# Performance work log

Hardware: AMD Instinct MI355X
Metric: run time of the kernel (lower is better)

## Reference

```python
import jax, jax.numpy as jnp
import numpy as np

N_NODES = 50000
N_EDGES = 1600000
IN_DIM = 128
N_HEADS = 8
OUT_DIM = 16  # output_dim // n_heads = 128 // 8


def setup_inputs() -> dict:
    key = jax.random.key(0)
    ks = jax.random.split(key, 8)
    feature = jax.random.normal(ks[0], (N_NODES, IN_DIM), dtype=jnp.float32)
    edge_src = jax.random.randint(ks[1], (N_EDGES,), 0, N_NODES)
    edge_dst = jax.random.randint(ks[2], (N_EDGES,), 0, N_NODES)
    edge_weight = jax.random.uniform(ks[3], (N_EDGES,), dtype=jnp.float32)
    w_lin = jax.random.normal(ks[4], (IN_DIM, N_HEADS * OUT_DIM), dtype=jnp.float32) * 0.1
    att_l = jax.random.normal(ks[5], (N_HEADS, OUT_DIM), dtype=jnp.float32) * 0.1
    att_r = jax.random.normal(ks[6], (N_HEADS, OUT_DIM), dtype=jnp.float32) * 0.1
    w_res = jax.random.normal(ks[7], (IN_DIM, N_HEADS * OUT_DIM), dtype=jnp.float32) * 0.1
    return {"feature": feature, "edge_src": edge_src, "edge_dst": edge_dst,
            "edge_weight": edge_weight, "w_lin": w_lin, "att_l": att_l,
            "att_r": att_r, "w_res": w_res}


def reference(feature, edge_src, edge_dst, edge_weight, w_lin, att_l, att_r, w_res):
    N = feature.shape[0]
    H, C = att_l.shape
    # Linear projection -> [N, H, C]
    x = (feature @ w_lin).reshape(N, H, C)
    # Per-node attention logits [N, H]
    al = jnp.einsum('nhc,hc->nh', x, att_l)
    ar = jnp.einsum('nhc,hc->nh', x, att_r)
    # Per-edge logits: gather src/dst, weight, leaky-relu  [E, H]
    alpha = al[edge_src] + ar[edge_dst]
    alpha = edge_weight[:, None] * alpha
    alpha = jax.nn.leaky_relu(alpha, negative_slope=0.2)
    # Segment softmax over edges grouped by destination node
    m = jax.ops.segment_max(alpha, edge_dst, num_segments=N)  # [N, H]
    m = jnp.where(jnp.isfinite(m), m, 0.0)
    e = jnp.exp(alpha - m[edge_dst])
    denom = jax.ops.segment_sum(e, edge_dst, num_segments=N)  # [N, H]
    coef = e / denom[edge_dst]                                 # [E, H]
    # Message passing: gather src feats, weight by coef, scatter-sum to dst
    msg = x[edge_src] * coef[:, :, None]                       # [E, H, C]
    feat = jax.ops.segment_sum(msg, edge_dst, num_segments=N)  # [N, H, C]
    out = jax.nn.elu(feat).reshape(N, H * C)
    out = out + feature @ w_res  # residual branch
    return out
```

## Files before the change

### kernel.cpp

```cpp
#include <hip/hip_runtime.h>
#include <math.h>

#define IN_DIM 128
#define NH 8
#define OC 16
#define HC 128
#define BSTR 136
#define ECH 4096
#define NBINS_MAX 512

typedef __attribute__((ext_vector_type(8))) short short8;
typedef __attribute__((ext_vector_type(4))) float f32x4;

__device__ __forceinline__ unsigned short bf16_rne(float f) {
  unsigned int u = __builtin_bit_cast(unsigned int, f);
  u += 0x7FFFu + ((u >> 16) & 1u);
  return (unsigned short)(u >> 16);
}
__device__ __forceinline__ float bf16_to_f(unsigned short h) {
  unsigned int u = ((unsigned int)h) << 16;
  return __builtin_bit_cast(float, u);
}

__global__ __launch_bounds__(256) void k1_fused(const float* __restrict__ feature,
                                                const float* __restrict__ w_lin,
                                                const float* __restrict__ w_res,
                                                unsigned short* __restrict__ xbf,
                                                float* __restrict__ out, int N) {
  __shared__ unsigned short BL[HC * BSTR];
  __shared__ unsigned short BR[HC * BSTR];
  const int t = threadIdx.x;
  for (int i = t; i < IN_DIM * HC; i += 256) {
    const int r = i >> 7, c = i & 127;
    BL[c * BSTR + r] = bf16_rne(w_lin[i]);
    BR[c * BSTR + r] = bf16_rne(w_res[i]);
  }
  __syncthreads();

  const int wave = t >> 6, lane = t & 63;
  const int n16 = lane & 15, quad = lane >> 4;
  const int nStrips = (N + 15) >> 4;

  for (int strip = blockIdx.x * 4 + wave; strip < nStrips; strip += gridDim.x * 4) {
    const int row0 = strip * 16;
    const int arow = row0 + n16;
    const float* __restrict__ ap =
        feature + (size_t)((arow < N) ? arow : 0) * IN_DIM + quad * 8;
    short8 ahi[4], alo[4];
#pragma unroll
    for (int ks = 0; ks < 4; ++ks) {
      const float4 f0 = *(const float4*)(ap + ks * 32);
      const float4 f1 = *(const float4*)(ap + ks * 32 + 4);
      const float fv[8] = {f0.x, f0.y, f0.z, f0.w, f1.x, f1.y, f1.z, f1.w};
      short8 h, l;
#pragma unroll
      for (int j = 0; j < 8; ++j) {
        const unsigned short hh = bf16_rne(fv[j]);
        h[j] = (short)hh;
        l[j] = (short)bf16_rne(fv[j] - bf16_to_f(hh));
      }
      ahi[ks] = h;
      alo[ks] = l;
    }
#pragma unroll
    for (int cg = 0; cg < 2; ++cg) {
      f32x4 acc[4] = {{0.f,0.f,0.f,0.f},{0.f,0.f,0.f,0.f},{0.f,0.f,0.f,0.f},{0.f,0.f,0.f,0.f}};
#pragma unroll
      for (int ks = 0; ks < 4; ++ks) {
#pragma unroll
        for (int j = 0; j < 4; ++j) {
          const int boff = ((cg * 4 + j) * 16 + n16) * BSTR + ks * 32 + quad * 8;
          const short8 bh = *(const short8*)&BL[boff];
          acc[j] = __builtin_amdgcn_mfma_f32_16x16x32_bf16(ahi[ks], bh, acc[j], 0, 0, 0);
          acc[j] = __builtin_amdgcn_mfma_f32_16x16x32_bf16(alo[ks], bh, acc[j], 0, 0, 0);
        }
      }
#pragma unroll
      for (int j = 0; j < 4; ++j) {
        const int colo = (cg * 4 + j) * 16 + n16;
#pragma unroll
        for (int r = 0; r < 4; ++r) {
          const int rr = row0 + quad * 4 + r;
          if (rr < N) xbf[(size_t)rr * HC + colo] = bf16_rne(acc[j][r]);
        }
      }
    }
#pragma unroll
    for (int cg = 0; cg < 2; ++cg) {
      f32x4 acc[4] = {{0.f,0.f,0.f,0.f},{0.f,0.f,0.f,0.f},{0.f,0.f,0.f,0.f},{0.f,0.f,0.f,0.f}};
#pragma unroll
      for (int ks = 0; ks < 4; ++ks) {
#pragma unroll
        for (int j = 0; j < 4; ++j) {
          const int boff = ((cg * 4 + j) * 16 + n16) * BSTR + ks * 32 + quad * 8;
          const short8 bh = *(const short8*)&BR[boff];
          acc[j] = __builtin_amdgcn_mfma_f32_16x16x32_bf16(ahi[ks], bh, acc[j], 0, 0, 0);
          acc[j] = __builtin_amdgcn_mfma_f32_16x16x32_bf16(alo[ks], bh, acc[j], 0, 0, 0);
        }
      }
#pragma unroll
      for (int j = 0; j < 4; ++j) {
        const int colo = (cg * 4 + j) * 16 + n16;
#pragma unroll
        for (int r = 0; r < 4; ++r) {
          const int rr = row0 + quad * 4 + r;
          if (rr < N) out[(size_t)rr * HC + colo] = acc[j][r];
        }
      }
    }
  }
}

__global__ __launch_bounds__(256) void k1b_attn(const unsigned short* __restrict__ xbf,
                                                const float* __restrict__ att_l,
                                                const float* __restrict__ att_r,
                                                float* __restrict__ al,
                                                float* __restrict__ ar,
                                                unsigned char* __restrict__ x8,
                                                float* __restrict__ s, int N) {
  const int idx = blockIdx.x * 256 + threadIdx.x;
  if (idx >= N * NH) return;
  const int h = idx & (NH - 1);
  const int n = idx >> 3;
  const ushort4* xp = (const ushort4*)(xbf + (size_t)idx * OC);
  const float4* lp = (const float4*)(att_l + h * OC);
  const float4* rp = (const float4*)(att_r + h * OC);
  float f[16];
  float sl = 0.f, sr = 0.f, m = 0.f;
#pragma unroll
  for (int q = 0; q < 4; ++q) {
    const ushort4 xu = xp[q];
    const float4 lv = lp[q], rv = rp[q];
    f[q * 4 + 0] = bf16_to_f(xu.x);
    f[q * 4 + 1] = bf16_to_f(xu.y);
    f[q * 4 + 2] = bf16_to_f(xu.z);
    f[q * 4 + 3] = bf16_to_f(xu.w);
    sl += f[q*4+0] * lv.x + f[q*4+1] * lv.y + f[q*4+2] * lv.z + f[q*4+3] * lv.w;
    sr += f[q*4+0] * rv.x + f[q*4+1] * rv.y + f[q*4+2] * rv.z + f[q*4+3] * rv.w;
#pragma unroll
    for (int j = 0; j < 4; ++j) m = fmaxf(m, fabsf(f[q * 4 + j]));
  }
  al[idx] = sl;
  ar[idx] = sr;
  m = fmaxf(m, __shfl_xor(m, 1, 64));
  m = fmaxf(m, __shfl_xor(m, 2, 64));
  m = fmaxf(m, __shfl_xor(m, 4, 64));
  const float inv = (m > 0.f) ? 127.f / m : 0.f;
  int4 pk;
  unsigned* pw = (unsigned*)&pk;
#pragma unroll
  for (int w = 0; w < 4; ++w) {
    unsigned b0 = (unsigned)((int)rintf(f[w * 4 + 0] * inv) + 128);
    unsigned b1 = (unsigned)((int)rintf(f[w * 4 + 1] * inv) + 128);
    unsigned b2 = (unsigned)((int)rintf(f[w * 4 + 2] * inv) + 128);
    unsigned b3 = (unsigned)((int)rintf(f[w * 4 + 3] * inv) + 128);
    pw[w] = (b0 & 0xFFu) | ((b1 & 0xFFu) << 8) | ((b2 & 0xFFu) << 16) | ((b3 & 0xFFu) << 24);
  }
  *(int4*)(x8 + (size_t)n * HC + h * 16) = pk;
  if (h == 0) s[n] = (m > 0.f) ? m / 127.f : 0.f;
}

__global__ __launch_bounds__(256) void kb1_scatter(const int* __restrict__ esrc,
                                                   const int* __restrict__ edst,
                                                   const float* __restrict__ ew,
                                                   int* __restrict__ bin_cursor,
                                                   uint2* __restrict__ tmp,
                                                   int E, int nbins, int cap) {
  __shared__ int cnt[NBINS_MAX];
  __shared__ int gbase[NBINS_MAX];
  const int t = threadIdx.x;
  cnt[t] = 0;
  cnt[t + 256] = 0;
  __syncthreads();
  const int base = blockIdx.x * ECH;
  uint2 v[16];
  int bj[16], sj[16];
#pragma unroll
  for (int j = 0; j < 16; ++j) {
    const int e = base + j * 256 + t;
    bj[j] = -1;
    if (e < E) {
      const int d = edst[e];
      v[j] = make_uint2((unsigned)esrc[e] | ((unsigned)(d & 127) << 16),
                        __float_as_uint(ew[e]));
      bj[j] = d >> 7;
      sj[j] = atomicAdd(&cnt[bj[j]], 1);
    }
  }
  __syncthreads();
  for (int b = t; b < nbins; b += 256) {
    const int own = cnt[b];
    if (own > 0) gbase[b] = atomicAdd(&bin_cursor[b], own);
  }
  __syncthreads();
#pragma unroll
  for (int j = 0; j < 16; ++j)
    if (bj[j] >= 0) {
      const int p = gbase[bj[j]] + sj[j];
      if (p < cap) tmp[(size_t)bj[j] * cap + p] = v[j];
    }
}

__global__ __launch_bounds__(512) void kb2_scan(const int* __restrict__ bin_cursor,
                                                int* __restrict__ bin_ofs,
                                                int* __restrict__ row_start,
                                                int nbins, int N) {
  __shared__ int s[512];
  const int t = threadIdx.x;
  const int own = (t < nbins) ? bin_cursor[t] : 0;
  s[t] = own;
  __syncthreads();
  for (int o = 1; o < 512; o <<= 1) {
    const int a = (t >= o) ? s[t - o] : 0;
    __syncthreads();
    s[t] += a;
    __syncthreads();
  }
  if (t < nbins) bin_ofs[t] = s[t] - own;
  if (t == nbins - 1) {
    bin_ofs[nbins] = s[t];
    row_start[N] = s[t];
  }
}

__global__ __launch_bounds__(256) void kb3_sort(const uint2* __restrict__ tmp,
                                                const int* __restrict__ bin_cursor,
                                                const int* __restrict__ bin_ofs,
                                                uint2* __restrict__ packed,
                                                int* __restrict__ row_start,
                                                int cap, int N) {
  const int b = blockIdx.x, t = threadIdx.x;
  const int M = bin_cursor[b];
  const int gstart = bin_ofs[b];
  const uint2* __restrict__ src = tmp + (size_t)b * cap;
  __shared__ int cnt[128];
  __shared__ int cur[128];
  __shared__ int s[128];
  if (t < 128) cnt[t] = 0;
  __syncthreads();
  for (int i = t; i < M; i += 256) atomicAdd(&cnt[src[i].x >> 16], 1);
  __syncthreads();
  if (t < 128) s[t] = cnt[t];
  __syncthreads();
  for (int o = 1; o < 128; o <<= 1) {
    int a = 0;
    if (t < 128 && t >= o) a = s[t - o];
    __syncthreads();
    if (t < 128) s[t] += a;
    __syncthreads();
  }
  if (t < 128) {
    const int ex = s[t] - cnt[t];
    cur[t] = gstart + ex;
    const int node = b * 128 + t;
    if (node < N) row_start[node] = gstart + ex;
  }
  __syncthreads();
  for (int i = t; i < M; i += 256) {
    const uint2 v = src[i];
    const int pos = atomicAdd(&cur[v.x >> 16], 1);
    packed[pos] = make_uint2(v.x & 0xFFFFu, v.y);
  }
}

__global__ __launch_bounds__(64) void k5_agg(const unsigned char* __restrict__ x8,
                                             const float* __restrict__ s,
                                             const uint2* __restrict__ packed,
                                             const int* __restrict__ row_start,
                                             const float* __restrict__ al,
                                             const float* __restrict__ ar,
                                             float* __restrict__ out, int N) {
  const int n = blockIdx.x;
  const int l = threadIdx.x;
  const int s0 = row_start[n];
  const int En = row_start[n + 1] - s0;
  if (En == 0) return;
  __shared__ int sbuf[64];
  __shared__ float wbuf[64];
  __shared__ float scbuf[64];
  const int h = l & 7;
  const int g = l >> 3;
  const int ch0 = h * 16;

  const float arn = ar[(size_t)n * NH + h];
  float dpart = 0.f;
  float facsum = 0.f;
  float f[16];
#pragma unroll
  for (int j = 0; j < 16; ++j) f[j] = 0.f;

  for (int base = 0; base < En; base += 64) {
    const int cnt = min(64, En - base);
    __syncthreads();
    if (l < cnt) {
      const uint2 p = packed[s0 + base + l];
      const int src = (int)p.x;
      sbuf[l] = src;
      wbuf[l] = __uint_as_float(p.y);
      scbuf[l] = s[src];
    }
    __syncthreads();
    for (int i = g; i < cnt; i += 8) {
      const int src = sbuf[i];
      float a = wbuf[i] * (al[(size_t)src * NH + h] + arn);
      a = (a > 0.f) ? a : 0.2f * a;
      const float e = __expf(a);
      dpart += e;
      const float fac = e * scbuf[i];
      facsum += fac;
      const int4 qw = *(const int4*)(x8 + (size_t)src * HC + ch0);
      const unsigned ux = (unsigned)qw.x, uy = (unsigned)qw.y;
      const unsigned uz = (unsigned)qw.z, uw = (unsigned)qw.w;
      f[0]  = fmaf(fac, (float)(ux & 0xFFu),         f[0]);
      f[1]  = fmaf(fac, (float)((ux >> 8) & 0xFFu),  f[1]);
      f[2]  = fmaf(fac, (float)((ux >> 16) & 0xFFu), f[2]);
      f[3]  = fmaf(fac, (float)(ux >> 24),           f[3]);
      f[4]  = fmaf(fac, (float)(uy & 0xFFu),         f[4]);
      f[5]  = fmaf(fac, (float)((uy >> 8) & 0xFFu),  f[5]);
      f[6]  = fmaf(fac, (float)((uy >> 16) & 0xFFu), f[6]);
      f[7]  = fmaf(fac, (float)(uy >> 24),           f[7]);
      f[8]  = fmaf(fac, (float)(uz & 0xFFu),         f[8]);
      f[9]  = fmaf(fac, (float)((uz >> 8) & 0xFFu),  f[9]);
      f[10] = fmaf(fac, (float)((uz >> 16) & 0xFFu), f[10]);
      f[11] = fmaf(fac, (float)(uz >> 24),           f[11]);
      f[12] = fmaf(fac, (float)(uw & 0xFFu),         f[12]);
      f[13] = fmaf(fac, (float)((uw >> 8) & 0xFFu),  f[13]);
      f[14] = fmaf(fac, (float)((uw >> 16) & 0xFFu), f[14]);
      f[15] = fmaf(fac, (float)(uw >> 24),           f[15]);
    }
  }
  dpart += __shfl_xor(dpart, 8);
  dpart += __shfl_xor(dpart, 16);
  dpart += __shfl_xor(dpart, 32);
  facsum += __shfl_xor(facsum, 8);
  facsum += __shfl_xor(facsum, 16);
  facsum += __shfl_xor(facsum, 32);
  const float inv = 1.f / dpart;
#pragma unroll
  for (int j = 0; j < 16; ++j) {
    f[j] += __shfl_xor(f[j], 8);
    f[j] += __shfl_xor(f[j], 16);
    f[j] += __shfl_xor(f[j], 32);
  }
  if (g == 0) {
    float* __restrict__ outp = out + (size_t)n * HC + ch0;
#pragma unroll
    for (int j = 0; j < 16; ++j) {
      const float feat = (f[j] - 128.f * facsum) * inv;
      const float o = (feat > 0.f) ? feat : (__expf(feat) - 1.f);
      outp[j] += o;
    }
  }
}

extern "C" void kernel_launch(void* const* d_in, const int* in_sizes, int n_in,
                              void* d_out, int out_size, void* d_ws, size_t ws_size,
                              hipStream_t stream) {
  const float* feature = (const float*)d_in[0];
  const int* esrc = (const int*)d_in[1];
  const int* edst = (const int*)d_in[2];
  const float* ew = (const float*)d_in[3];
  const float* w_lin = (const float*)d_in[4];
  const float* att_l = (const float*)d_in[5];
  const float* att_r = (const float*)d_in[6];
  const float* w_res = (const float*)d_in[7];
  float* out = (float*)d_out;

  const int N = in_sizes[0] / IN_DIM;
  const int E = in_sizes[1];
  const int nbins = (N + 127) >> 7;
  int cap = (E + nbins - 1) / nbins;
  cap = cap + cap / 4 + 512;
  cap = (cap + 63) & ~63;
  const int nch = (E + ECH - 1) / ECH;

  char* ws = (char*)d_ws;
  size_t off = 0;
  auto alloc = [&](size_t bytes) {
    void* p = ws + off;
    off = (off + bytes + 255) & ~(size_t)255;
    return p;
  };
  const size_t xbf_bytes = (size_t)N * HC * sizeof(unsigned short);
  const size_t tmp_bytes = (size_t)nbins * cap * sizeof(uint2);
  void* region0 = alloc(tmp_bytes > xbf_bytes ? tmp_bytes : xbf_bytes);
  unsigned short* xbf = (unsigned short*)region0;
  uint2* tmp = (uint2*)region0;

  unsigned char* x8 = (unsigned char*)alloc((size_t)N * HC);
  float* sscale = (float*)alloc((size_t)N * sizeof(float));
  float* al = (float*)alloc((size_t)N * NH * sizeof(float));
  float* ar = (float*)alloc((size_t)N * NH * sizeof(float));
  int* row_start = (int*)alloc((size_t)(N + 1) * sizeof(int));
  int* bin_cursor = (int*)alloc((size_t)NBINS_MAX * sizeof(int));
  int* bin_ofs = (int*)alloc((size_t)(NBINS_MAX + 1) * sizeof(int));
  uint2* packed = (uint2*)alloc((size_t)E * sizeof(uint2));

  hipMemsetAsync(bin_cursor, 0, (size_t)NBINS_MAX * sizeof(int), stream);
  k1_fused<<<512, 256, 0, stream>>>(feature, w_lin, w_res, xbf, out, N);
  k1b_attn<<<(N * NH + 255) / 256, 256, 0, stream>>>(xbf, att_l, att_r, al, ar, x8, sscale, N);
  kb1_scatter<<<nch, 256, 0, stream>>>(esrc, edst, ew, bin_cursor, tmp, E, nbins, cap);
  kb2_scan<<<1, 512, 0, stream>>>(bin_cursor, bin_ofs, row_start, nbins, N);
  kb3_sort<<<nbins, 256, 0, stream>>>(tmp, bin_cursor, bin_ofs, packed, row_start, cap, N);
  k5_agg<<<N, 64, 0, stream>>>(x8, sscale, packed, row_start, al, ar, out, N);
}
```

Before: 223.9 us.

## Fuse attention logits and int8 quantization into GEMM kernel, drop scan and memset launches

The projection GEMM now computes the per-node attention logits and the per-node int8 quantization straight from the MFMA accumulators, so the bf16 intermediate and the separate attention kernel go away. The bin-cursor memset moves into block 0 of the GEMM kernel. The single-block scan kernel is replaced by each sort block summing the preceding bin counts itself. The aggregation epilogue now reduces partial sums through shared memory and writes float2 vectors instead of using shuffles and a single-group store. Together this removes several launches and an HBM round trip, at the cost of more shuffles in the GEMM and redundant prefix sums in the sort kernel. The memset now relies on the GEMM kernel finishing before the scatter kernel starts.

```diff
diff --git a/kernel.cpp b/kernel.cpp
--- a/kernel.cpp
+++ b/kernel.cpp
@@ -8,6 +8,7 @@
 #define BSTR 136
 #define ECH 4096
 #define NBINS_MAX 512
+#define FSTR 132
 
 typedef __attribute__((ext_vector_type(8))) short short8;
 typedef __attribute__((ext_vector_type(4))) float f32x4;
@@ -25,11 +26,21 @@
 __global__ __launch_bounds__(256) void k1_fused(const float* __restrict__ feature,
                                                 const float* __restrict__ w_lin,
                                                 const float* __restrict__ w_res,
-                                                unsigned short* __restrict__ xbf,
-                                                float* __restrict__ out, int N) {
+                                                const float* __restrict__ att_l,
+                                                const float* __restrict__ att_r,
+                                                unsigned char* __restrict__ x8,
+                                                float* __restrict__ sscale,
+                                                float* __restrict__ al,
+                                                float* __restrict__ ar,
+                                                float* __restrict__ out,
+                                                int* __restrict__ bin_cursor, int N) {
   __shared__ unsigned short BL[HC * BSTR];
   __shared__ unsigned short BR[HC * BSTR];
   const int t = threadIdx.x;
+  if (blockIdx.x == 0) {
+    bin_cursor[t] = 0;
+    bin_cursor[t + 256] = 0;
+  }
   for (int i = t; i < IN_DIM * HC; i += 256) {
     const int r = i >> 7, c = i & 127;
     BL[c * BSTR + r] = bf16_rne(w_lin[i]);
@@ -39,6 +50,12 @@
 
   const int wave = t >> 6, lane = t & 63;
   const int n16 = lane & 15, quad = lane >> 4;
+  float attl[8], attr[8];
+#pragma unroll
+  for (int hh = 0; hh < 8; ++hh) {
+    attl[hh] = att_l[hh * OC + n16];
+    attr[hh] = att_r[hh * OC + n16];
+  }
   const int nStrips = (N + 15) >> 4;
 
   for (int strip = blockIdx.x * 4 + wave; strip < nStrips; strip += gridDim.x * 4) {
@@ -62,26 +79,62 @@
       ahi[ks] = h;
       alo[ks] = l;
     }
-#pragma unroll
-    for (int cg = 0; cg < 2; ++cg) {
-      f32x4 acc[4] = {{0.f,0.f,0.f,0.f},{0.f,0.f,0.f,0.f},{0.f,0.f,0.f,0.f},{0.f,0.f,0.f,0.f}};
-#pragma unroll
-      for (int ks = 0; ks < 4; ++ks) {
-#pragma unroll
-        for (int j = 0; j < 4; ++j) {
-          const int boff = ((cg * 4 + j) * 16 + n16) * BSTR + ks * 32 + quad * 8;
-          const short8 bh = *(const short8*)&BL[boff];
-          acc[j] = __builtin_amdgcn_mfma_f32_16x16x32_bf16(ahi[ks], bh, acc[j], 0, 0, 0);
-          acc[j] = __builtin_amdgcn_mfma_f32_16x16x32_bf16(alo[ks], bh, acc[j], 0, 0, 0);
+    f32x4 xacc[8];
+#pragma unroll
+    for (int u = 0; u < 8; ++u) xacc[u] = (f32x4){0.f, 0.f, 0.f, 0.f};
+#pragma unroll
+    for (int ks = 0; ks < 4; ++ks) {
+#pragma unroll
+      for (int u = 0; u < 8; ++u) {
+        const int boff = (u * 16 + n16) * BSTR + ks * 32 + quad * 8;
+        const short8 bh = *(const short8*)&BL[boff];
+        xacc[u] = __builtin_amdgcn_mfma_f32_16x16x32_bf16(ahi[ks], bh, xacc[u], 0, 0, 0);
+        xacc[u] = __builtin_amdgcn_mfma_f32_16x16x32_bf16(alo[ks], bh, xacc[u], 0, 0, 0);
+      }
+    }
+    float m[4];
+#pragma unroll
+    for (int r = 0; r < 4; ++r) {
+      float mm = 0.f;
+#pragma unroll
+      for (int u = 0; u < 8; ++u) mm = fmaxf(mm, fabsf(xacc[u][r]));
+      mm = fmaxf(mm, __shfl_xor(mm, 1));
+      mm = fmaxf(mm, __shfl_xor(mm, 2));
+      mm = fmaxf(mm, __shfl_xor(mm, 4));
+      mm = fmaxf(mm, __shfl_xor(mm, 8));
+      m[r] = mm;
+    }
+#pragma unroll
+    for (int r = 0; r < 4; ++r) {
+      const int rr = row0 + quad * 4 + r;
+      if (rr < N) {
+        const float inv = (m[r] > 0.f) ? 127.f / m[r] : 0.f;
+#pragma unroll
+        for (int u = 0; u < 8; ++u) {
+          const int q8 = (int)rintf(xacc[u][r] * inv) + 128;
+          x8[(size_t)rr * HC + u * 16 + n16] = (unsigned char)q8;
         }
-      }
-#pragma unroll
-      for (int j = 0; j < 4; ++j) {
-        const int colo = (cg * 4 + j) * 16 + n16;
-#pragma unroll
-        for (int r = 0; r < 4; ++r) {
-          const int rr = row0 + quad * 4 + r;
-          if (rr < N) xbf[(size_t)rr * HC + colo] = bf16_rne(acc[j][r]);
+        if (n16 == 0) sscale[rr] = (m[r] > 0.f) ? m[r] / 127.f : 0.f;
+      }
+    }
+#pragma unroll
+    for (int u = 0; u < 8; ++u) {
+#pragma unroll
+      for (int r = 0; r < 4; ++r) {
+        float tl = xacc[u][r] * attl[u];
+        float tr = xacc[u][r] * attr[u];
+        tl += __shfl_xor(tl, 1);
+        tr += __shfl_xor(tr, 1);
+        tl += __shfl_xor(tl, 2);
+        tr += __shfl_xor(tr, 2);
+        tl += __shfl_xor(tl, 4);
+        tr += __shfl_xor(tr, 4);
+        tl += __shfl_xor(tl, 8);
+        tr += __shfl_xor(tr, 8);
+        const int rr = row0 + quad * 4 + r;
+        if (n16 == 0 && rr < N) {
+          al[(size_t)rr * NH + u] = tl;
+          ar[(size_t)rr * NH + u] = tr;
         }
       }
     }
@@ -109,55 +162,6 @@
       }
     }
   }
-}
-
-__global__ __launch_bounds__(256) void k1b_attn(const unsigned short* __restrict__ xbf,
-                                                const float* __restrict__ att_l,
-                                                const float* __restrict__ att_r,
-                                                float* __restrict__ al,
-                                                float* __restrict__ ar,
-                                                unsigned char* __restrict__ x8,
-                                                float* __restrict__ s, int N) {
-  const int idx = blockIdx.x * 256 + threadIdx.x;
-  if (idx >= N * NH) return;
-  const int h = idx & (NH - 1);
-  const int n = idx >> 3;
-  const ushort4* xp = (const ushort4*)(xbf + (size_t)idx * OC);
-  const float4* lp = (const float4*)(att_l + h * OC);
-  const float4* rp = (const float4*)(att_r + h * OC);
-  float f[16];
-  float sl = 0.f, sr = 0.f, m = 0.f;
-#pragma unroll
-  for (int q = 0; q < 4; ++q) {
-    const ushort4 xu = xp[q];
-    const float4 lv = lp[q], rv = rp[q];
-    f[q * 4 + 0] = bf16_to_f(xu.x);
-    f[q * 4 + 1] = bf16_to_f(xu.y);
-    f[q * 4 + 2] = bf16_to_f(xu.z);
-    f[q * 4 + 3] = bf16_to_f(xu.w);
-    sl += f[q*4+0] * lv.x + f[q*4+1] * lv.y + f[q*4+2] * lv.z + f[q*4+3] * lv.w;
-    sr += f[q*4+0] * rv.x + f[q*4+1] * rv.y + f[q*4+2] * rv.z + f[q*4+3] * rv.w;
-#pragma unroll
-    for (int j = 0; j < 4; ++j) m = fmaxf(m, fabsf(f[q * 4 + j]));
-  }
-  al[idx] = sl;
-  ar[idx] = sr;
-  m = fmaxf(m, __shfl_xor(m, 1, 64));
-  m = fmaxf(m, __shfl_xor(m, 2, 64));
-  m = fmaxf(m, __shfl_xor(m, 4, 64));
-  const float inv = (m > 0.f) ? 127.f / m : 0.f;
-  int4 pk;
-  unsigned* pw = (unsigned*)&pk;
-#pragma unroll
-  for (int w = 0; w < 4; ++w) {
-    unsigned b0 = (unsigned)((int)rintf(f[w * 4 + 0] * inv) + 128);
-    unsigned b1 = (unsigned)((int)rintf(f[w * 4 + 1] * inv) + 128);
-    unsigned b2 = (unsigned)((int)rintf(f[w * 4 + 2] * inv) + 128);
-    unsigned b3 = (unsigned)((int)rintf(f[w * 4 + 3] * inv) + 128);
-    pw[w] = (b0 & 0xFFu) | ((b1 & 0xFFu) << 8) | ((b2 & 0xFFu) << 16) | ((b3 & 0xFFu) << 24);
-  }
-  *(int4*)(x8 + (size_t)n * HC + h * 16) = pk;
-  if (h == 0) s[n] = (m > 0.f) ? m / 127.f : 0.f;
 }
 
 __global__ __launch_bounds__(256) void kb1_scatter(const int* __restrict__ esrc,
@@ -197,41 +201,27 @@
   for (int j = 0; j < 16; ++j)
     if (bj[j] >= 0) {
       const int p = gbase[bj[j]] + sj[j];
-      if (p < cap) tmp[(size_t)bj[j] * cap + p] = v[j];
-    }
-}
-
-__global__ __launch_bounds__(512) void kb2_scan(const int* __restrict__ bin_cursor,
-                                                int* __restrict__ bin_ofs,
-                                                int* __restrict__ row_start,
-                                                int nbins, int N) {
-  __shared__ int s[512];
-  const int t = threadIdx.x;
-  const int own = (t < nbins) ? bin_cursor[t] : 0;
-  s[t] = own;
-  __syncthreads();
-  for (int o = 1; o < 512; o <<= 1) {
-    const int a = (t >= o) ? s[t - o] : 0;
-    __syncthreads();
-    s[t] += a;
-    __syncthreads();
-  }
-  if (t < nbins) bin_ofs[t] = s[t] - own;
-  if (t == nbins - 1) {
-    bin_ofs[nbins] = s[t];
-    row_start[N] = s[t];
-  }
+      if (p >= 0 && p < cap) tmp[(size_t)bj[j] * cap + p] = v[j];
+    }
 }
 
 __global__ __launch_bounds__(256) void kb3_sort(const uint2* __restrict__ tmp,
                                                 const int* __restrict__ bin_cursor,
-                                                const int* __restrict__ bin_ofs,
                                                 uint2* __restrict__ packed,
                                                 int* __restrict__ row_start,
-                                                int cap, int N) {
+                                                int cap, int nbins, int N) {
   const int b = blockIdx.x, t = threadIdx.x;
   const int M = bin_cursor[b];
-  const int gstart = bin_ofs[b];
+  __shared__ int redw[4];
+  int part = 0;
+  for (int i = t; i < b; i += 256) part += bin_cursor[i];
+#pragma unroll
+  for (int o = 32; o >= 1; o >>= 1) part += __shfl_xor(part, o);
+  if ((t & 63) == 0) redw[t >> 6] = part;
+  __syncthreads();
+  const int gstart = redw[0] + redw[1] + redw[2] + redw[3];
+  if (b == nbins - 1 && t == 0) row_start[N] = gstart + M;
+
   const uint2* __restrict__ src = tmp + (size_t)b * cap;
   __shared__ int cnt[128];
   __shared__ int cur[128];
@@ -278,6 +268,7 @@
   __shared__ int sbuf[64];
   __shared__ float wbuf[64];
   __shared__ float scbuf[64];
+  __shared__ float fred[8 * FSTR];
   const int h = l & 7;
   const int g = l >> 3;
   const int ch0 = h * 16;
@@ -335,22 +326,30 @@
   facsum += __shfl_xor(facsum, 8);
   facsum += __shfl_xor(facsum, 16);
   facsum += __shfl_xor(facsum, 32);
-  const float inv = 1.f / dpart;
-#pragma unroll
-  for (int j = 0; j < 16; ++j) {
-    f[j] += __shfl_xor(f[j], 8);
-    f[j] += __shfl_xor(f[j], 16);
-    f[j] += __shfl_xor(f[j], 32);
-  }
-  if (g == 0) {
-    float* __restrict__ outp = out + (size_t)n * HC + ch0;
-#pragma unroll
-    for (int j = 0; j < 16; ++j) {
-      const float feat = (f[j] - 128.f * facsum) * inv;
-      const float o = (feat > 0.f) ? feat : (__expf(feat) - 1.f);
-      outp[j] += o;
-    }
-  }
+#pragma unroll
+  for (int q = 0; q < 4; ++q) {
+    const f32x4 v = {f[q * 4 + 0], f[q * 4 + 1], f[q * 4 + 2], f[q * 4 + 3]};
+    *(f32x4*)&fred[g * FSTR + ch0 + q * 4] = v;
+  }
+  __syncthreads();
+  float a0 = 0.f, a1 = 0.f;
+#pragma unroll
+  for (int gg = 0; gg < 8; ++gg) {
+    const float2 v = *(const float2*)&fred[gg * FSTR + 2 * l];
+    a0 += v.x;
+    a1 += v.y;
+  }
+  const float dH = __shfl(dpart, l >> 3);
+  const float fsH = __shfl(facsum, l >> 3);
+  const float inv = 1.f / dH;
+  float f0 = (a0 - 128.f * fsH) * inv;
+  float f1 = (a1 - 128.f * fsH) * inv;
+  f0 = (f0 > 0.f) ? f0 : (__expf(f0) - 1.f);
+  f1 = (f1 > 0.f) ? f1 : (__expf(f1) - 1.f);
+  float2 o = *(float2*)&out[(size_t)n * HC + 2 * l];
+  o.x += f0;
+  o.y += f1;
+  *(float2*)&out[(size_t)n * HC + 2 * l] = o;
 }
 
 extern "C" void kernel_launch(void* const* d_in, const int* in_sizes, int n_in,
@@ -381,26 +380,18 @@
     off = (off + bytes + 255) & ~(size_t)255;
     return p;
   };
-  const size_t xbf_bytes = (size_t)N * HC * sizeof(unsigned short);
-  const size_t tmp_bytes = (size_t)nbins * cap * sizeof(uint2);
-  void* region0 = alloc(tmp_bytes > xbf_bytes ? tmp_bytes : xbf_bytes);
-  unsigned short* xbf = (unsigned short*)region0;
-  uint2* tmp = (uint2*)region0;
-
+  uint2* tmp = (uint2*)alloc((size_t)nbins * cap * sizeof(uint2));
   unsigned char* x8 = (unsigned char*)alloc((size_t)N * HC);
   float* sscale = (float*)alloc((size_t)N * sizeof(float));
   float* al = (float*)alloc((size_t)N * NH * sizeof(float));
   float* ar = (float*)alloc((size_t)N * NH * sizeof(float));
   int* row_start = (int*)alloc((size_t)(N + 1) * sizeof(int));
   int* bin_cursor = (int*)alloc((size_t)NBINS_MAX * sizeof(int));
-  int* bin_ofs = (int*)alloc((size_t)(NBINS_MAX + 1) * sizeof(int));
   uint2* packed = (uint2*)alloc((size_t)E * sizeof(uint2));
 
-  hipMemsetAsync(bin_cursor, 0, (size_t)NBINS_MAX * sizeof(int), stream);
-  k1_fused<<<512, 256, 0, stream>>>(feature, w_lin, w_res, xbf, out, N);
-  k1b_attn<<<(N * NH + 255) / 256, 256, 0, stream>>>(xbf, att_l, att_r, al, ar, x8, sscale, N);
+  k1_fused<<<512, 256, 0, stream>>>(feature, w_lin, w_res, att_l, att_r,
+                                    x8, sscale, al, ar, out, bin_cursor, N);
   kb1_scatter<<<nch, 256, 0, stream>>>(esrc, edst, ew, bin_cursor, tmp, E, nbins, cap);
-  kb2_scan<<<1, 512, 0, stream>>>(bin_cursor, bin_ofs, row_start, nbins, N);
-  kb3_sort<<<nbins, 256, 0, stream>>>(tmp, bin_cursor, bin_ofs, packed, row_start, cap, N);
+  kb3_sort<<<nbins, 256, 0, stream>>>(tmp, bin_cursor, packed, row_start, cap, nbins, N);
   k5_agg<<<N, 64, 0, stream>>>(x8, sscale, packed, row_start, al, ar, out, N);
 }
```

Result: faster. 204.0 us (-8.9%).
